# Kernel optimization log

Measured on AMD Instinct MI355X. Metric: run time of the kernel, lower is better.

## Reference

```python
import jax, jax.numpy as jnp
import numpy as np

NUM_HEADS = 8
NUM_GROUPS = 32
EPS = 1e-5


def setup_inputs() -> dict:
    key = jax.random.key(0)
    ks = jax.random.split(key, 7)
    B, C, H, W = 8, 512, 32, 32
    x = jax.random.normal(ks[0], (B, C, H, W), dtype=jnp.float32)
    # GroupNorm affine params
    gn_w = jnp.ones((C,), dtype=jnp.float32)
    gn_b = jnp.zeros((C,), dtype=jnp.float32)
    # 1x1 conv == linear over channel dim; store squeezed weights (out, in)
    qkv_w = jax.random.normal(ks[1], (3 * C, C), dtype=jnp.float32) * (1.0 / np.sqrt(C))
    qkv_b = jnp.zeros((3 * C,), dtype=jnp.float32)
    proj_w = jax.random.normal(ks[2], (C, C), dtype=jnp.float32) * (1.0 / np.sqrt(C))
    proj_b = jnp.zeros((C,), dtype=jnp.float32)
    return {"x": x, "gn_w": gn_w, "gn_b": gn_b, "qkv_w": qkv_w,
            "qkv_b": qkv_b, "proj_w": proj_w, "proj_b": proj_b}


def reference(x, gn_w, gn_b, qkv_w, qkv_b, proj_w, proj_b):
    B, C, H, W = x.shape
    G = NUM_GROUPS
    hd = C // NUM_HEADS
    scale = hd ** -0.5
    # GroupNorm: normalize over (C//G, H, W) per group
    xg = x.reshape(B, G, C // G, H, W)
    mean = xg.mean(axis=(2, 3, 4), keepdims=True)
    var = xg.var(axis=(2, 3, 4), keepdims=True)
    xn = ((xg - mean) * jax.lax.rsqrt(var + EPS)).reshape(B, C, H, W)
    xn = xn * gn_w[None, :, None, None] + gn_b[None, :, None, None]
    # QKV 1x1 conv
    qkv = jnp.einsum('bchw,oc->bohw', xn, qkv_w) + qkv_b[None, :, None, None]
    # (B, 3, heads, head_dim, HW) -> (3, B, heads, HW, head_dim)
    qkv = qkv.reshape(B, 3, NUM_HEADS, hd, H * W).transpose(1, 0, 2, 4, 3)
    q, k, v = qkv[0], qkv[1], qkv[2]
    attn = jax.nn.softmax(jnp.einsum('bhqd,bhkd->bhqk', q, k) * scale, axis=-1)
    out = jnp.einsum('bhqk,bhkd->bhqd', attn, v)  # (B, heads, HW, hd)
    out = out.transpose(0, 1, 3, 2).reshape(B, C, H, W)
    out = jnp.einsum('bchw,oc->bohw', out, proj_w) + proj_b[None, :, None, None]
    return out + x
```

## Files before the change

kernel.cpp:

```cpp
#include <hip/hip_runtime.h>
#include <hip/hip_bf16.h>
#include <math.h>

typedef __bf16 bf16_t;
typedef __bf16 bf16x8 __attribute__((ext_vector_type(8)));
typedef __bf16 bf16x4 __attribute__((ext_vector_type(4)));
typedef float  f32x4  __attribute__((ext_vector_type(4)));
typedef short  short4v __attribute__((ext_vector_type(4)));

#define NB    8
#define NC    512
#define NHW   1024
#define NHEAD 8
#define NHD   64
#define NG    32
#define NCG   16
#define NO3   1536

__device__ __forceinline__ void lds_load16(bf16_t* lds, const bf16_t* g) {
  __builtin_amdgcn_global_load_lds(
      (__attribute__((address_space(1))) unsigned int*)(g),
      (__attribute__((address_space(3))) unsigned int*)(void*)(lds),
      16, 0, 0);
}

__device__ __forceinline__ f32x4 mfma16(bf16x4 a, bf16x4 b, f32x4 c) {
#if __has_builtin(__builtin_amdgcn_mfma_f32_16x16x16bf16_1k)
  return __builtin_amdgcn_mfma_f32_16x16x16bf16_1k(
      __builtin_bit_cast(short4v, a), __builtin_bit_cast(short4v, b), c, 0, 0, 0);
#else
  f32x4 d;
  asm("v_mfma_f32_16x16x16_bf16 %0, %1, %2, %3"
      : "=v"(d) : "v"(a), "v"(b), "v"(c));
  return d;
#endif
}

__global__ __launch_bounds__(256)
void gn_kernel(const float* __restrict__ x, const float* __restrict__ gw,
               const float* __restrict__ gb, bf16_t* __restrict__ xn)
{
  const int bg = blockIdx.x;
  const int b = bg >> 5, g = bg & 31;
  const float* xp = x + ((size_t)b * NC + g * NCG) * NHW;
  const int tid = threadIdx.x;
  const int wave = tid >> 6, lane = tid & 63;

  float s1 = 0.f, s2 = 0.f;
  const float4* xp4 = (const float4*)xp;
  for (int i = tid; i < 4096; i += 256) {
    float4 v = xp4[i];
    s1 += v.x + v.y + v.z + v.w;
    s2 += v.x * v.x + v.y * v.y + v.z * v.z + v.w * v.w;
  }
  for (int off = 32; off > 0; off >>= 1) {
    s1 += __shfl_down(s1, off);
    s2 += __shfl_down(s2, off);
  }
  __shared__ float red[16];
  if (lane == 0) { red[wave] = s1; red[8 + wave] = s2; }
  __syncthreads();
  float tot1 = red[0] + red[1] + red[2] + red[3];
  float tot2 = red[8] + red[9] + red[10] + red[11];
  const float mean = tot1 * (1.0f / 16384.0f);
  const float var  = tot2 * (1.0f / 16384.0f) - mean * mean;
  const float rstd = rsqrtf(var + 1e-5f);

  float gam[NCG], bet[NCG];
  #pragma unroll
  for (int c = 0; c < NCG; ++c) {
    gam[c] = gw[g * NCG + c] * rstd;
    bet[c] = gb[g * NCG + c] - mean * gam[c];
  }
  bf16_t* op = xn + (size_t)b * NHW * NC + g * NCG;
  for (int s = tid; s < NHW; s += 256) {
    __align__(16) bf16_t vals[NCG];
    #pragma unroll
    for (int c = 0; c < NCG; ++c)
      vals[c] = (bf16_t)(xp[c * NHW + s] * gam[c] + bet[c]);
    *(bf16x8*)(op + (size_t)s * NC)     = *(const bf16x8*)&vals[0];
    *(bf16x8*)(op + (size_t)s * NC + 8) = *(const bf16x8*)&vals[8];
  }
}

__global__ __launch_bounds__(256)
void wconv_kernel(const float* __restrict__ qw, const float* __restrict__ pw,
                  bf16_t* __restrict__ qwb, bf16_t* __restrict__ pwb)
{
  const int gid = blockIdx.x * 256 + threadIdx.x;
  const int n1 = NO3 * NC / 4;
  float4 v; bf16x4 o;
  if (gid < n1) {
    v = ((const float4*)qw)[gid];
    o[0] = (bf16_t)v.x; o[1] = (bf16_t)v.y; o[2] = (bf16_t)v.z; o[3] = (bf16_t)v.w;
    ((bf16x4*)qwb)[gid] = o;
  } else {
    int g2 = gid - n1;
    v = ((const float4*)pw)[g2];
    o[0] = (bf16_t)v.x; o[1] = (bf16_t)v.y; o[2] = (bf16_t)v.z; o[3] = (bf16_t)v.w;
    ((bf16x4*)pwb)[g2] = o;
  }
}

__device__ __forceinline__ void gemm_mainloop(const bf16_t* Ap, const bf16_t* Bp,
                                              bf16_t* sA, bf16_t* sB, f32x4 (&acc)[4][4])
{
  const int tid = threadIdx.x;
  const int wave = tid >> 6, lane = tid & 63;
  const int quad = lane >> 4, l16 = lane & 15;
  const int wm = wave >> 1, wn = wave & 1;
  for (int k0 = 0; k0 < 512; k0 += 32) {
    #pragma unroll
    for (int j = 0; j < 2; ++j) {
      int c = wave * 64 + j * 256 + lane;
      int row = c >> 2, ko = (c & 3) * 8;
      lds_load16(sA + (size_t)(wave * 64 + j * 256) * 8, Ap + (size_t)row * 512 + k0 + ko);
      lds_load16(sB + (size_t)(wave * 64 + j * 256) * 8, Bp + (size_t)row * 512 + k0 + ko);
    }
    __syncthreads();
    bf16x8 af[4], bfr[4];
    #pragma unroll
    for (int mi = 0; mi < 4; ++mi)
      af[mi] = *(const bf16x8*)(sA + (wm * 64 + mi * 16 + l16) * 32 + quad * 8);
    #pragma unroll
    for (int ni = 0; ni < 4; ++ni)
      bfr[ni] = *(const bf16x8*)(sB + (wn * 64 + ni * 16 + l16) * 32 + quad * 8);
    #pragma unroll
    for (int mi = 0; mi < 4; ++mi)
      #pragma unroll
      for (int ni = 0; ni < 4; ++ni)
        acc[mi][ni] = __builtin_amdgcn_mfma_f32_16x16x32_bf16(af[mi], bfr[ni], acc[mi][ni], 0, 0, 0);
    __syncthreads();
  }
}

__global__ __launch_bounds__(256, 2)
void qkv_gemm(const bf16_t* __restrict__ xn, const bf16_t* __restrict__ w,
              const float* __restrict__ bias,
              bf16_t* __restrict__ qbuf, bf16_t* __restrict__ kbuf, bf16_t* __restrict__ vbuf)
{
  __shared__ __align__(16) bf16_t smem[128 * 136];
  bf16_t* sA = smem;
  bf16_t* sB = smem + 4096;
  const int tid = threadIdx.x;
  const int wave = tid >> 6, lane = tid & 63;
  const int quad = lane >> 4, l16 = lane & 15;
  const int wm = wave >> 1, wn = wave & 1;
  const int bx = blockIdx.x, by = blockIdx.y, b = blockIdx.z;

  const bf16_t* Ap = xn + ((size_t)b * NHW + by * 128) * NC;
  const bf16_t* Bp = w + (size_t)bx * 128 * NC;
  f32x4 acc[4][4] = {};
  gemm_mainloop(Ap, Bp, sA, sB, acc);

  const int obase = bx * 128 + wn * 64;
  const int sbase = by * 128 + wm * 64;
  float bv[4];
  #pragma unroll
  for (int ni = 0; ni < 4; ++ni) bv[ni] = bias[obase + ni * 16 + l16];

  if (bx < 8) {
    const bool isq = (bx < 4);
    bf16_t* basep = isq ? qbuf : kbuf;
    const float scale = isq ? 0.125f : 1.0f;
    #pragma unroll
    for (int ni = 0; ni < 4; ++ni) {
      int o = obase + ni * 16 + l16;
      int hh = (o >> 6) & 7, dd = o & 63;
      bf16_t* dst = basep + ((size_t)(b * NHEAD + hh) * NHW) * NHD + dd;
      #pragma unroll
      for (int mi = 0; mi < 4; ++mi)
        #pragma unroll
        for (int r = 0; r < 4; ++r) {
          int s = sbase + mi * 16 + quad * 4 + r;
          dst[(size_t)s * NHD] = (bf16_t)((acc[mi][ni][r] + bv[ni]) * scale);
        }
    }
  } else {
    bf16_t* sC = smem;
    __syncthreads();
    #pragma unroll
    for (int ni = 0; ni < 4; ++ni)
      #pragma unroll
      for (int mi = 0; mi < 4; ++mi)
        #pragma unroll
        for (int r = 0; r < 4; ++r)
          sC[(wn * 64 + ni * 16 + l16) * 136 + wm * 64 + mi * 16 + quad * 4 + r] =
              (bf16_t)(acc[mi][ni][r] + bv[ni]);
    __syncthreads();
    int o_local = tid >> 1, shalf = (tid & 1) << 6;
    int ov = (bx - 8) * 128 + o_local;
    int hh = ov >> 6, dd = ov & 63;
    bf16_t* dst = vbuf + ((size_t)(b * NHEAD + hh) * NHD + dd) * NHW + by * 128 + shalf;
    #pragma unroll
    for (int jj = 0; jj < 8; ++jj)
      *(bf16x8*)(dst + jj * 8) = *(const bf16x8*)&sC[o_local * 136 + shalf + jj * 8];
  }
}

__global__ __launch_bounds__(256, 2)
void attn_kernel(const bf16_t* __restrict__ qbuf, const bf16_t* __restrict__ kbuf,
                 const bf16_t* __restrict__ vbuf, bf16_t* __restrict__ obuf)
{
  __shared__ __align__(16) bf16_t Ks[128 * 72];
  __shared__ __align__(16) bf16_t Vs[64 * 136];

  const int tid = threadIdx.x;
  const int wave = tid >> 6, lane = tid & 63;
  const int quad = lane >> 4, l16 = lane & 15;
  const int idx = blockIdx.x;
  const int qt = idx & 7, h = (idx >> 3) & 7, b = idx >> 6;
  const size_t bh = (size_t)b * NHEAD + h;
  const bf16_t* qp = qbuf + (bh * NHW + qt * 128 + wave * 32) * NHD;
  const bf16_t* kp = kbuf + bh * NHW * NHD;
  const bf16_t* vp = vbuf + bh * NHD * NHW;

  bf16x8 qf[2][2];
  #pragma unroll
  for (int stile = 0; stile < 2; ++stile)
    #pragma unroll
    for (int kc = 0; kc < 2; ++kc)
      qf[stile][kc] = *(const bf16x8*)(qp + (size_t)(stile * 16 + l16) * NHD + kc * 32 + quad * 8);

  float m_i[2] = {-1e30f, -1e30f}, l_i[2] = {0.f, 0.f};
  f32x4 oacc[4][2] = {};

  for (int kt = 0; kt < 8; ++kt) {
    const bf16_t* ksrc = kp + (size_t)kt * 128 * NHD;
    const bf16_t* vsrc = vp + kt * 128;
    #pragma unroll
    for (int j = 0; j < 4; ++j) {
      int c = tid + j * 256;
      int t = c >> 3, doff = (c & 7) * 8;
      *(bf16x8*)&Ks[t * 72 + doff] = *(const bf16x8*)(ksrc + (size_t)t * NHD + doff);
    }
    #pragma unroll
    for (int j = 0; j < 4; ++j) {
      int c = tid + j * 256;
      int d = c >> 4, toff = (c & 15) * 8;
      *(bf16x8*)&Vs[d * 136 + toff] = *(const bf16x8*)(vsrc + (size_t)d * NHW + toff);
    }
    __syncthreads();

    f32x4 st[2][8];
    #pragma unroll
    for (int mt = 0; mt < 8; ++mt) {
      bf16x8 ka0 = *(const bf16x8*)&Ks[(mt * 16 + l16) * 72 + quad * 8];
      bf16x8 ka1 = *(const bf16x8*)&Ks[(mt * 16 + l16) * 72 + 32 + quad * 8];
      #pragma unroll
      for (int stile = 0; stile < 2; ++stile) {
        f32x4 z = {};
        z = __builtin_amdgcn_mfma_f32_16x16x32_bf16(ka0, qf[stile][0], z, 0, 0, 0);
        z = __builtin_amdgcn_mfma_f32_16x16x32_bf16(ka1, qf[stile][1], z, 0, 0, 0);
        st[stile][mt] = z;
      }
    }

    #pragma unroll
    for (int stile = 0; stile < 2; ++stile) {
      float mx = -1e30f;
      #pragma unroll
      for (int mt = 0; mt < 8; ++mt)
        #pragma unroll
        for (int r = 0; r < 4; ++r) mx = fmaxf(mx, st[stile][mt][r]);
      mx = fmaxf(mx, __shfl_xor(mx, 16));
      mx = fmaxf(mx, __shfl_xor(mx, 32));
      float mnew = fmaxf(m_i[stile], mx);
      float alpha = __expf(m_i[stile] - mnew);
      m_i[stile] = mnew;
      float rs = 0.f;
      #pragma unroll
      for (int mt = 0; mt < 8; ++mt)
        #pragma unroll
        for (int r = 0; r < 4; ++r) {
          float p = __expf(st[stile][mt][r] - mnew);
          rs += p;
          st[stile][mt][r] = p;
        }
      rs += __shfl_xor(rs, 16);
      rs += __shfl_xor(rs, 32);
      l_i[stile] = l_i[stile] * alpha + rs;
      #pragma unroll
      for (int mi = 0; mi < 4; ++mi)
        #pragma unroll
        for (int r = 0; r < 4; ++r)
          oacc[mi][stile][r] *= alpha;
    }

    #pragma unroll
    for (int mt = 0; mt < 8; ++mt) {
      bf16x4 pb[2];
      #pragma unroll
      for (int stile = 0; stile < 2; ++stile) {
        pb[stile][0] = (bf16_t)st[stile][mt][0];
        pb[stile][1] = (bf16_t)st[stile][mt][1];
        pb[stile][2] = (bf16_t)st[stile][mt][2];
        pb[stile][3] = (bf16_t)st[stile][mt][3];
      }
      #pragma unroll
      for (int mi = 0; mi < 4; ++mi) {
        bf16x4 va = *(const bf16x4*)&Vs[(mi * 16 + l16) * 136 + mt * 16 + quad * 4];
        oacc[mi][0] = mfma16(va, pb[0], oacc[mi][0]);
        oacc[mi][1] = mfma16(va, pb[1], oacc[mi][1]);
      }
    }
    __syncthreads();
  }

  #pragma unroll
  for (int stile = 0; stile < 2; ++stile) {
    float inv = 1.0f / l_i[stile];
    int s = qt * 128 + wave * 32 + stile * 16 + l16;
    bf16_t* orow = obuf + ((size_t)b * NHW + s) * NC + h * NHD;
    #pragma unroll
    for (int mi = 0; mi < 4; ++mi) {
      __align__(8) bf16_t o4[4];
      #pragma unroll
      for (int r = 0; r < 4; ++r) o4[r] = (bf16_t)(oacc[mi][stile][r] * inv);
      *(bf16x4*)(orow + mi * 16 + quad * 4) = *(const bf16x4*)o4;
    }
  }
}

__global__ __launch_bounds__(256, 2)
void proj_gemm(const bf16_t* __restrict__ ob, const bf16_t* __restrict__ w,
               const float* __restrict__ bias, const float* __restrict__ x,
               float* __restrict__ out)
{
  __shared__ __align__(16) bf16_t smem[8192];
  bf16_t* sA = smem;
  bf16_t* sB = smem + 4096;
  const int tid = threadIdx.x;
  const int wave = tid >> 6, lane = tid & 63;
  const int quad = lane >> 4, l16 = lane & 15;
  const int wm = wave >> 1, wn = wave & 1;
  const int bx = blockIdx.x, by = blockIdx.y, b = blockIdx.z;

  const bf16_t* Ap = w + (size_t)by * 128 * NC;
  const bf16_t* Bp = ob + ((size_t)b * NHW + bx * 128) * NC;
  f32x4 acc[4][4] = {};
  gemm_mainloop(Ap, Bp, sA, sB, acc);

  const int cobase = by * 128 + wm * 64;
  const int sbase  = bx * 128 + wn * 64;
  #pragma unroll
  for (int mi = 0; mi < 4; ++mi)
    #pragma unroll
    for (int r = 0; r < 4; ++r) {
      int co = cobase + mi * 16 + quad * 4 + r;
      float pb = bias[co];
      const float* xrow = x + ((size_t)b * NC + co) * NHW;
      float* orow = out + ((size_t)b * NC + co) * NHW;
      #pragma unroll
      for (int ni = 0; ni < 4; ++ni) {
        int s = sbase + ni * 16 + l16;
        orow[s] = acc[mi][ni][r] + pb + xrow[s];
      }
    }
}

extern "C" void kernel_launch(void* const* d_in, const int* in_sizes, int n_in,
                              void* d_out, int out_size, void* d_ws, size_t ws_size,
                              hipStream_t stream)
{
  const float* x      = (const float*)d_in[0];
  const float* gn_w   = (const float*)d_in[1];
  const float* gn_b   = (const float*)d_in[2];
  const float* qkv_w  = (const float*)d_in[3];
  const float* qkv_b  = (const float*)d_in[4];
  const float* proj_w = (const float*)d_in[5];
  const float* proj_b = (const float*)d_in[6];
  float* out = (float*)d_out;

  char* ws = (char*)d_ws;
  bf16_t* xn   = (bf16_t*)(ws);
  bf16_t* qwb  = (bf16_t*)(ws + 8388608);
  bf16_t* pwb  = (bf16_t*)(ws + 9961472);
  bf16_t* qbuf = (bf16_t*)(ws + 10485760);
  bf16_t* kbuf = (bf16_t*)(ws + 18874368);
  bf16_t* vbuf = (bf16_t*)(ws + 27262976);
  bf16_t* obuf = xn;

  gn_kernel<<<dim3(NB * NG), dim3(256), 0, stream>>>(x, gn_w, gn_b, xn);
  wconv_kernel<<<dim3(1024), dim3(256), 0, stream>>>(qkv_w, proj_w, qwb, pwb);
  qkv_gemm<<<dim3(12, 8, NB), dim3(256), 0, stream>>>(xn, qwb, qkv_b, qbuf, kbuf, vbuf);
  attn_kernel<<<dim3(512), dim3(256), 0, stream>>>(qbuf, kbuf, vbuf, obuf);
  proj_gemm<<<dim3(8, 4, NB), dim3(256), 0, stream>>>(obuf, pwb, proj_b, x, out);
}
```

Measured before the change: 174.3 us.

## Split attention keys across two wave groups with register prefetch and exp2 softmax

The attention kernel goes from 256 to 512 threads. The two groups of four waves each take half of every 128-key tile, and their partial softmax states are merged through shared memory at the end. The next K/V tile is prefetched into registers while the current one is being computed, and the softmax switches to exp2, with log2(e) folded into the Q scale in the QKV GEMM. The block index mapping is also reordered so batch varies fastest. The costs are an extra merge pass through LDS, extra barriers, and more register pressure under launch_bounds(512,4).

```diff
diff --git a/kernel.cpp b/kernel.cpp
--- a/kernel.cpp
+++ b/kernel.cpp
@@ -162,7 +162,7 @@
   if (bx < 8) {
     const bool isq = (bx < 4);
     bf16_t* basep = isq ? qbuf : kbuf;
-    const float scale = isq ? 0.125f : 1.0f;
+    const float scale = isq ? 0.18033688f : 1.0f;
     #pragma unroll
     for (int ni = 0; ni < 4; ++ni) {
       int o = obase + ni * 16 + l16;
@@ -198,20 +198,27 @@
   }
 }
 
-__global__ __launch_bounds__(256, 2)
+__global__ __launch_bounds__(512, 4)
 void attn_kernel(const bf16_t* __restrict__ qbuf, const bf16_t* __restrict__ kbuf,
                  const bf16_t* __restrict__ vbuf, bf16_t* __restrict__ obuf)
 {
-  __shared__ __align__(16) bf16_t Ks[128 * 72];
-  __shared__ __align__(16) bf16_t Vs[64 * 136];
+  __shared__ __align__(16) char smem_raw[36864];
+  bf16_t* Ks = (bf16_t*)smem_raw;
+  bf16_t* Vs = (bf16_t*)(smem_raw + 18432);
+  f32x4*  mO = (f32x4*)smem_raw;
+  float*  mM = (float*)(smem_raw + 32768);
+  float*  mL = mM + 512;
 
   const int tid = threadIdx.x;
   const int wave = tid >> 6, lane = tid & 63;
   const int quad = lane >> 4, l16 = lane & 15;
+  const int wl = wave & 3;
+  const int wg = wave >> 2;
+  const int mtb = wg * 4;
   const int idx = blockIdx.x;
-  const int qt = idx & 7, h = (idx >> 3) & 7, b = idx >> 6;
+  const int qt = idx >> 6, h = (idx >> 3) & 7, b = idx & 7;
   const size_t bh = (size_t)b * NHEAD + h;
-  const bf16_t* qp = qbuf + (bh * NHW + qt * 128 + wave * 32) * NHD;
+  const bf16_t* qp = qbuf + (bh * NHW + qt * 128 + wl * 32) * NHD;
   const bf16_t* kp = kbuf + bh * NHW * NHD;
   const bf16_t* vp = vbuf + bh * NHD * NHW;
 
@@ -225,28 +232,44 @@
   float m_i[2] = {-1e30f, -1e30f}, l_i[2] = {0.f, 0.f};
   f32x4 oacc[4][2] = {};
 
+  bf16x8 kreg[2], vreg[2];
+  {
+    const bf16_t* ksrc = kp;
+    const bf16_t* vsrc = vp;
+    #pragma unroll
+    for (int j = 0; j < 2; ++j) {
+      int c = tid + j * 512;
+      kreg[j] = *(const bf16x8*)(ksrc + (size_t)(c >> 3) * NHD + (c & 7) * 8);
+      vreg[j] = *(const bf16x8*)(vsrc + (size_t)(c >> 4) * NHW + (c & 15) * 8);
+    }
+  }
+
   for (int kt = 0; kt < 8; ++kt) {
-    const bf16_t* ksrc = kp + (size_t)kt * 128 * NHD;
-    const bf16_t* vsrc = vp + kt * 128;
-    #pragma unroll
-    for (int j = 0; j < 4; ++j) {
-      int c = tid + j * 256;
-      int t = c >> 3, doff = (c & 7) * 8;
-      *(bf16x8*)&Ks[t * 72 + doff] = *(const bf16x8*)(ksrc + (size_t)t * NHD + doff);
-    }
-    #pragma unroll
-    for (int j = 0; j < 4; ++j) {
-      int c = tid + j * 256;
-      int d = c >> 4, toff = (c & 15) * 8;
-      *(bf16x8*)&Vs[d * 136 + toff] = *(const bf16x8*)(vsrc + (size_t)d * NHW + toff);
-    }
-    __syncthreads();
-
-    f32x4 st[2][8];
-    #pragma unroll
-    for (int mt = 0; mt < 8; ++mt) {
-      bf16x8 ka0 = *(const bf16x8*)&Ks[(mt * 16 + l16) * 72 + quad * 8];
-      bf16x8 ka1 = *(const bf16x8*)&Ks[(mt * 16 + l16) * 72 + 32 + quad * 8];
+    __syncthreads();
+    #pragma unroll
+    for (int j = 0; j < 2; ++j) {
+      int c = tid + j * 512;
+      *(bf16x8*)&Ks[(c >> 3) * 72 + (c & 7) * 8]  = kreg[j];
+      *(bf16x8*)&Vs[(c >> 4) * 136 + (c & 15) * 8] = vreg[j];
+    }
+    __syncthreads();
+    if (kt < 7) {
+      const bf16_t* ksrc = kp + (size_t)(kt + 1) * 128 * NHD;
+      const bf16_t* vsrc = vp + (kt + 1) * 128;
+      #pragma unroll
+      for (int j = 0; j < 2; ++j) {
+        int c = tid + j * 512;
+        kreg[j] = *(const bf16x8*)(ksrc + (size_t)(c >> 3) * NHD + (c & 7) * 8);
+        vreg[j] = *(const bf16x8*)(vsrc + (size_t)(c >> 4) * NHW + (c & 15) * 8);
+      }
+    }
+
+    f32x4 st[2][4];
+    #pragma unroll
+    for (int mt = 0; mt < 4; ++mt) {
+      int mtg = mtb + mt;
+      bf16x8 ka0 = *(const bf16x8*)&Ks[(mtg * 16 + l16) * 72 + quad * 8];
+      bf16x8 ka1 = *(const bf16x8*)&Ks[(mtg * 16 + l16) * 72 + 32 + quad * 8];
       #pragma unroll
       for (int stile = 0; stile < 2; ++stile) {
         f32x4 z = {};
@@ -260,20 +283,20 @@
     for (int stile = 0; stile < 2; ++stile) {
       float mx = -1e30f;
       #pragma unroll
-      for (int mt = 0; mt < 8; ++mt)
+      for (int mt = 0; mt < 4; ++mt)
         #pragma unroll
         for (int r = 0; r < 4; ++r) mx = fmaxf(mx, st[stile][mt][r]);
       mx = fmaxf(mx, __shfl_xor(mx, 16));
       mx = fmaxf(mx, __shfl_xor(mx, 32));
       float mnew = fmaxf(m_i[stile], mx);
-      float alpha = __expf(m_i[stile] - mnew);
+      float alpha = exp2f(m_i[stile] - mnew);
       m_i[stile] = mnew;
       float rs = 0.f;
       #pragma unroll
-      for (int mt = 0; mt < 8; ++mt)
+      for (int mt = 0; mt < 4; ++mt)
         #pragma unroll
         for (int r = 0; r < 4; ++r) {
-          float p = __expf(st[stile][mt][r] - mnew);
+          float p = exp2f(st[stile][mt][r] - mnew);
           rs += p;
           st[stile][mt][r] = p;
         }
@@ -288,7 +311,8 @@
     }
 
     #pragma unroll
-    for (int mt = 0; mt < 8; ++mt) {
+    for (int mt = 0; mt < 4; ++mt) {
+      int mtg = mtb + mt;
       bf16x4 pb[2];
       #pragma unroll
       for (int stile = 0; stile < 2; ++stile) {
@@ -299,25 +323,45 @@
       }
       #pragma unroll
       for (int mi = 0; mi < 4; ++mi) {
-        bf16x4 va = *(const bf16x4*)&Vs[(mi * 16 + l16) * 136 + mt * 16 + quad * 4];
+        bf16x4 va = *(const bf16x4*)&Vs[(mi * 16 + l16) * 136 + mtg * 16 + quad * 4];
         oacc[mi][0] = mfma16(va, pb[0], oacc[mi][0]);
         oacc[mi][1] = mfma16(va, pb[1], oacc[mi][1]);
       }
     }
-    __syncthreads();
-  }
-
-  #pragma unroll
-  for (int stile = 0; stile < 2; ++stile) {
-    float inv = 1.0f / l_i[stile];
-    int s = qt * 128 + wave * 32 + stile * 16 + l16;
-    bf16_t* orow = obuf + ((size_t)b * NHW + s) * NC + h * NHD;
-    #pragma unroll
-    for (int mi = 0; mi < 4; ++mi) {
-      __align__(8) bf16_t o4[4];
-      #pragma unroll
-      for (int r = 0; r < 4; ++r) o4[r] = (bf16_t)(oacc[mi][stile][r] * inv);
-      *(bf16x4*)(orow + mi * 16 + quad * 4) = *(const bf16x4*)o4;
+  }
+
+  __syncthreads();
+  if (wg == 1) {
+    #pragma unroll
+    for (int stile = 0; stile < 2; ++stile) {
+      mM[(wl * 2 + stile) * 64 + lane] = m_i[stile];
+      mL[(wl * 2 + stile) * 64 + lane] = l_i[stile];
+      #pragma unroll
+      for (int mi = 0; mi < 4; ++mi)
+        mO[((wl * 2 + stile) * 4 + mi) * 64 + lane] = oacc[mi][stile];
+    }
+  }
+  __syncthreads();
+  if (wg == 0) {
+    #pragma unroll
+    for (int stile = 0; stile < 2; ++stile) {
+      float mB = mM[(wl * 2 + stile) * 64 + lane];
+      float lB = mL[(wl * 2 + stile) * 64 + lane];
+      float mS = fmaxf(m_i[stile], mB);
+      float aA = exp2f(m_i[stile] - mS);
+      float aB = exp2f(mB - mS);
+      float inv = 1.0f / (l_i[stile] * aA + lB * aB);
+      int s = qt * 128 + wl * 32 + stile * 16 + l16;
+      bf16_t* orow = obuf + ((size_t)b * NHW + s) * NC + h * NHD;
+      #pragma unroll
+      for (int mi = 0; mi < 4; ++mi) {
+        f32x4 oB = mO[((wl * 2 + stile) * 4 + mi) * 64 + lane];
+        __align__(8) bf16_t o4[4];
+        #pragma unroll
+        for (int r = 0; r < 4; ++r)
+          o4[r] = (bf16_t)((oacc[mi][stile][r] * aA + oB[r] * aB) * inv);
+        *(bf16x4*)(orow + mi * 16 + quad * 4) = *(const bf16x4*)o4;
+      }
     }
   }
 }
@@ -384,6 +428,6 @@
   gn_kernel<<<dim3(NB * NG), dim3(256), 0, stream>>>(x, gn_w, gn_b, xn);
   wconv_kernel<<<dim3(1024), dim3(256), 0, stream>>>(qkv_w, proj_w, qwb, pwb);
   qkv_gemm<<<dim3(12, 8, NB), dim3(256), 0, stream>>>(xn, qwb, qkv_b, qbuf, kbuf, vbuf);
-  attn_kernel<<<dim3(512), dim3(256), 0, stream>>>(qbuf, kbuf, vbuf, obuf);
+  attn_kernel<<<dim3(512), dim3(512), 0, stream>>>(qbuf, kbuf, vbuf, obuf);
   proj_gemm<<<dim3(8, 4, NB), dim3(256), 0, stream>>>(obuf, pwb, proj_b, x, out);
 }
```

Result: no change. 171.3 us (-1.7%).
